# Performance work log

Hardware: AMD Instinct MI355X
Metric: run time of the kernel (lower is better)

Reference implementation:

```python
import jax, jax.numpy as jnp
import numpy as np

B, WIN, NN, NF, NH, NOUT = 4, 10, 10000, 8, 64, 1
N = B * WIN * NN          # stacked graph nodes
E = 3200000               # edges
EPS = 1e-5                # BatchNorm eps


def _gcn(x, edge_index, ew, W, b):
    # PyG GCNConv: linear first, then sym-normalized aggregation with self loops.
    xl = x @ W  # [N, H]
    loop = jnp.arange(N)
    row = jnp.concatenate([edge_index[0], loop])
    col = jnp.concatenate([edge_index[1], loop])
    w = jnp.concatenate([ew, jnp.ones((N,), ew.dtype)])
    deg = jax.ops.segment_sum(w, col, num_segments=N)
    dinv = jnp.where(deg > 0, jax.lax.rsqrt(deg), 0.0)
    norm = dinv[row] * w * dinv[col]
    out = jax.ops.segment_sum(norm[:, None] * xl[row], col, num_segments=N)
    return out + b


def _bn(x, g, bta):
    # training-mode BatchNorm1d (batch statistics, biased variance)
    m = x.mean(0)
    v = x.var(0)
    return (x - m) * jax.lax.rsqrt(v + EPS) * g + bta


def _lstm(xs, wih, whh, bih, bhh):
    # xs: [T, Bn, D]; PyTorch gate order i, f, g, o
    H = whh.shape[1]
    Bn = xs.shape[1]
    h0 = jnp.zeros((Bn, H), xs.dtype)
    c0 = jnp.zeros((Bn, H), xs.dtype)
    def step(carry, xt):
        h, c = carry
        gates = xt @ wih.T + bih + h @ whh.T + bhh
        i, f, g, o = jnp.split(gates, 4, axis=-1)
        c = jax.nn.sigmoid(f) * c + jax.nn.sigmoid(i) * jnp.tanh(g)
        h = jax.nn.sigmoid(o) * jnp.tanh(c)
        return (h, c), h
    (hn, cn), ys = jax.lax.scan(step, (h0, c0), xs)
    return ys, hn


def setup_inputs() -> dict:
    key = jax.random.key(0)
    ks = jax.random.split(key, 16)
    def rn(k, shape, s=0.05):
        return jax.random.normal(k, shape, jnp.float32) * s
    return {
        "x": jax.random.normal(ks[0], (N, NF), jnp.float32),
        "edge_index": jax.random.randint(ks[1], (2, E), 0, N),
        "edge_weight": jax.random.uniform(ks[2], (E,), jnp.float32),
        "c1_w": rn(ks[3], (NF, NH)), "c1_b": jnp.zeros((NH,), jnp.float32),
        "c2_w": rn(ks[4], (NH, NH)), "c2_b": jnp.zeros((NH,), jnp.float32),
        "bn1_g": jnp.ones((NH,), jnp.float32), "bn1_b": jnp.zeros((NH,), jnp.float32),
        "bn2_g": jnp.ones((NH,), jnp.float32), "bn2_b": jnp.zeros((NH,), jnp.float32),
        "l1_wih": rn(ks[5], (4 * NH, 2 * NH)), "l1_whh": rn(ks[6], (4 * NH, NH)),
        "l1_bih": jnp.zeros((4 * NH,), jnp.float32), "l1_bhh": jnp.zeros((4 * NH,), jnp.float32),
        "l2_wih": rn(ks[7], (4 * NH, NH)), "l2_whh": rn(ks[8], (4 * NH, NH)),
        "l2_bih": jnp.zeros((4 * NH,), jnp.float32), "l2_bhh": jnp.zeros((4 * NH,), jnp.float32),
        "fc1_w": rn(ks[9], (NH, 2 * NH + WIN * NF)), "fc1_b": jnp.zeros((NH,), jnp.float32),
        "fc2_w": rn(ks[10], (NOUT, NH)), "fc2_b": jnp.zeros((NOUT,), jnp.float32),
    }


def reference(x, edge_index, edge_weight, c1_w, c1_b, c2_w, c2_b,
              bn1_g, bn1_b, bn2_g, bn2_b,
              l1_wih, l1_whh, l1_bih, l1_bhh,
              l2_wih, l2_whh, l2_bih, l2_bhh,
              fc1_w, fc1_b, fc2_w, fc2_b):
    # skip connection: raw features per (batch,node) over the window
    skip = x.reshape(B, WIN, NN, NF).transpose(0, 2, 1, 3).reshape(B * NN, WIN * NF)
    # two GCN layers (dropout is identity in deterministic/eval reference)
    h1 = _bn(jax.nn.relu(_gcn(x, edge_index, edge_weight, c1_w, c1_b)), bn1_g, bn1_b)
    h2 = _bn(jax.nn.relu(_gcn(h1, edge_index, edge_weight, c2_w, c2_b)), bn2_g, bn2_b)
    xc = jnp.concatenate([h1, h2], axis=1)  # [N, 2H]
    xr = xc.reshape(B, WIN, NN, 2 * NH).transpose(1, 0, 2, 3).reshape(WIN, B * NN, 2 * NH)
    ys1, hn1 = _lstm(xr, l1_wih, l1_whh, l1_bih, l1_bhh)
    ys2, hn2 = _lstm(ys1, l2_wih, l2_whh, l2_bih, l2_bhh)
    z = jnp.concatenate([hn1, hn2, skip], axis=1)
    z = jax.nn.relu(z @ fc1_w.T + fc1_b)
    z = jax.nn.relu(z @ fc2_w.T + fc2_b)
    return z.reshape(-1)
```

## Files before the change

kernel.cpp:

```cpp
#include <hip/hip_runtime.h>
#include <math.h>

constexpr int BB     = 4;
constexpr int WINN   = 10;
constexpr int NNODES = 10000;
constexpr int NFEAT  = 8;
constexpr int NHID   = 64;
constexpr int NTOT   = BB * WINN * NNODES;
constexpr int NEDGE  = 3200000;
constexpr int NBN    = BB * NNODES;
constexpr float EPSBN = 1e-5f;

#define DEVFN static __device__ __forceinline__

typedef float f4 __attribute__((ext_vector_type(4)));
typedef short s8v __attribute__((ext_vector_type(8)));
typedef unsigned short ushort_t;
typedef unsigned int uint_t;

DEVFN float sigmoidf_(float x) { return 1.0f / (1.0f + __expf(-x)); }
DEVFN float tanhf_(float x) { return 2.0f / (1.0f + __expf(-2.0f * x)) - 1.0f; }
DEVFN ushort_t f2bf(float f) {
    uint_t x = __float_as_uint(f);
    return (ushort_t)((x + 0x7FFFu + ((x >> 16) & 1u)) >> 16);
}
DEVFN float bf2f(ushort_t u) { return __uint_as_float(((uint_t)u) << 16); }

__global__ void k_diag(float* out, float wsz, int n) {
    int i = blockIdx.x * 256 + threadIdx.x;
    if (i < n) out[i] = wsz;
}

__global__ void k_init(int* cntP, float* sums) {
    int i = blockIdx.x * 256 + threadIdx.x;
    if (i < 8 * NTOT) cntP[i] = 0;
    if (i < 2048) sums[i] = 0.f;
}

__global__ void k_hist(const int* __restrict__ ei, int* __restrict__ cntP) {
    int e = blockIdx.x * 256 + threadIdx.x;
    int p = blockIdx.x & 7;
    if (e < NEDGE) atomicAdd(&cntP[p * NTOT + ei[NEDGE + e]], 1);
}

__global__ void k_scan1(const int* __restrict__ cntP, int* __restrict__ ptr, int* __restrict__ tmp) {
    __shared__ int sdat[256];
    int tid = threadIdx.x;
    int base = blockIdx.x * 1024 + tid * 4;
    int v[4];
#pragma unroll
    for (int j = 0; j < 4; ++j) {
        int idx = base + j;
        int s = 0;
        if (idx < NTOT) {
#pragma unroll
            for (int p = 0; p < 8; ++p) s += cntP[p * NTOT + idx];
        }
        v[j] = s;
    }
    int sum = v[0] + v[1] + v[2] + v[3];
    sdat[tid] = sum;
    __syncthreads();
    for (int ofs = 1; ofs < 256; ofs <<= 1) {
        int x = (tid >= ofs) ? sdat[tid - ofs] : 0;
        __syncthreads();
        sdat[tid] += x;
        __syncthreads();
    }
    int run = sdat[tid] - sum;
    if (base + 0 < NTOT) ptr[base + 0] = run; run += v[0];
    if (base + 1 < NTOT) ptr[base + 1] = run; run += v[1];
    if (base + 2 < NTOT) ptr[base + 2] = run; run += v[2];
    if (base + 3 < NTOT) ptr[base + 3] = run;
    if (tid == 255) tmp[blockIdx.x] = sdat[255];
}

__global__ void k_scan2(int* tmp, int nb) {
    __shared__ int st[512];
    int tid = threadIdx.x;
    int v = (tid < nb) ? tmp[tid] : 0;
    st[tid] = v;
    __syncthreads();
    for (int ofs = 1; ofs < 512; ofs <<= 1) {
        int x = (tid >= ofs) ? st[tid - ofs] : 0;
        __syncthreads();
        st[tid] += x;
        __syncthreads();
    }
    if (tid < nb) tmp[tid] = st[tid] - v;
}

__global__ void k_scan3(int* __restrict__ ptr, int* __restrict__ cntP, const int* __restrict__ tmp) {
    int i = blockIdx.x * 256 + threadIdx.x;
    if (i < NTOT) {
        int p0 = ptr[i] + tmp[i >> 10];
        ptr[i] = p0;
        int run = p0;
#pragma unroll
        for (int p = 0; p < 8; ++p) {
            int c = cntP[p * NTOT + i];
            cntP[p * NTOT + i] = run;
            run += c;
        }
    }
    if (i == 0) ptr[NTOT] = NEDGE;
}

__global__ void k_fill(const int* __restrict__ ei, const float* __restrict__ ew,
                       int* __restrict__ cur8, int2* __restrict__ epack) {
    int e = blockIdx.x * 256 + threadIdx.x;
    if (e >= NEDGE) return;
    int p = blockIdx.x & 7;
    int row = ei[e], col = ei[NEDGE + e];
    int pos = atomicAdd(&cur8[p * NTOT + col], 1);
    epack[pos] = make_int2(row, __float_as_int(ew[e]));
}

__global__ void k_degcsr(const int* __restrict__ ptr, const int2* __restrict__ epack,
                         float* __restrict__ dinv) {
    int tid = threadIdx.x;
    int lane = tid & 63;
    int waveg = blockIdx.x * 4 + (tid >> 6);
    int g = lane >> 3, sub = lane & 7;
    int node = waveg * 8 + g;
    int beg = ptr[node], end = ptr[node + 1];
    float s = 0.f;
    for (int e = beg + sub; e < end; e += 8) s += __int_as_float(epack[e].y);
    s += __shfl_xor(s, 1, 64);
    s += __shfl_xor(s, 2, 64);
    s += __shfl_xor(s, 4, 64);
    if (sub == 0) dinv[node] = rsqrtf(1.0f + s);
}

__global__ void k_gather8(const int* __restrict__ ptr, const int2* __restrict__ epack,
                          const float* __restrict__ x, const float* __restrict__ dinv,
                          float* __restrict__ aggX) {
    int tid = threadIdx.x;
    int lane = tid & 63;
    int waveg = blockIdx.x * 4 + (tid >> 6);
    int g = lane >> 3, ch = lane & 7;
    int node = waveg * 8 + g;
    int beg = ptr[node], end = ptr[node + 1];
    float dv = dinv[node];
    float accE = 0.f;
    int e = beg;
    for (; e + 3 < end; e += 4) {
        int2 p0 = epack[e], p1 = epack[e + 1], p2 = epack[e + 2], p3 = epack[e + 3];
        float n0 = dinv[p0.x] * __int_as_float(p0.y);
        float n1 = dinv[p1.x] * __int_as_float(p1.y);
        float n2 = dinv[p2.x] * __int_as_float(p2.y);
        float n3 = dinv[p3.x] * __int_as_float(p3.y);
        accE = fmaf(n0, x[p0.x * 8 + ch], accE);
        accE = fmaf(n1, x[p1.x * 8 + ch], accE);
        accE = fmaf(n2, x[p2.x * 8 + ch], accE);
        accE = fmaf(n3, x[p3.x * 8 + ch], accE);
    }
    for (; e < end; ++e) {
        int2 p = epack[e];
        accE = fmaf(dinv[p.x] * __int_as_float(p.y), x[p.x * 8 + ch], accE);
    }
    aggX[node * 8 + ch] = dv * fmaf(dv, x[node * 8 + ch], accE);
}

__global__ void k_lin1(const float* __restrict__ aggX, const float* __restrict__ W,
                       const float* __restrict__ bias, ushort_t* __restrict__ rbf,
                       float* __restrict__ sums) {
    __shared__ float sW[NFEAT * NHID];
    int tid = threadIdx.x;
    sW[tid] = W[tid];
    sW[tid + 256] = W[tid + 256];
    __syncthreads();
    int c = tid & 63;
    float b = bias[c];
    float s = 0.f, sq = 0.f;
    int stride = gridDim.x * 256;
    for (int i = blockIdx.x * 256 + tid; i < NTOT * 64; i += stride) {
        int n = i >> 6;
        float acc = b;
#pragma unroll
        for (int f = 0; f < NFEAT; ++f) acc = fmaf(aggX[n * NFEAT + f], sW[f * NHID + c], acc);
        acc = acc > 0.f ? acc : 0.f;
        rbf[i] = f2bf(acc);
        s += acc;
        sq = fmaf(acc, acc, sq);
    }
    __shared__ float ls[4][64], lq[4][64];
    int w = tid >> 6;
    ls[w][c] = s; lq[w][c] = sq;
    __syncthreads();
    if (tid < 64) {
        atomicAdd(&sums[tid], ls[0][tid] + ls[1][tid] + ls[2][tid] + ls[3][tid]);
        atomicAdd(&sums[64 + tid], lq[0][tid] + lq[1][tid] + lq[2][tid] + lq[3][tid]);
    }
}

__global__ void k_bn_final(const float* __restrict__ sums, const float* __restrict__ g,
                           const float* __restrict__ b, float* __restrict__ ss) {
    int i = threadIdx.x;
    if (i >= 64) return;
    float mean = sums[i] * (1.0f / NTOT);
    float var = sums[64 + i] * (1.0f / NTOT) - mean * mean;
    float sc = g[i] * rsqrtf(var + EPSBN);
    ss[i] = sc;
    ss[64 + i] = b[i] - mean * sc;
}

__global__ void k_bn_final8(const float* __restrict__ sums8, const float* __restrict__ g,
                            const float* __restrict__ b, float* __restrict__ ss) {
    int i = threadIdx.x;
    if (i >= 64) return;
    float S = 0.f, Q = 0.f;
#pragma unroll
    for (int m = 0; m < 8; ++m) { S += sums8[m * 128 + i]; Q += sums8[m * 128 + 64 + i]; }
    float mean = S * (1.0f / NTOT);
    float var = Q * (1.0f / NTOT) - mean * mean;
    float sc = g[i] * rsqrtf(var + EPSBN);
    ss[i] = sc;
    ss[64 + i] = b[i] - mean * sc;
}

__global__ void k_gcn2(const int* __restrict__ ptr, const int2* __restrict__ epack,
                       const ushort_t* __restrict__ rbf, const float* __restrict__ dinv,
                       const float* __restrict__ ss1, const float* __restrict__ W2,
                       const float* __restrict__ bias2, ushort_t* __restrict__ h2bf,
                       float* __restrict__ sums8) {
    __shared__ __align__(16) float srow[4][64];
    __shared__ float ls[4][64], lq[4][64];
    int lane = threadIdx.x & 63, wv = threadIdx.x >> 6;
    float wc[64];
#pragma unroll
    for (int h = 0; h < 64; ++h) wc[h] = W2[h * 64 + lane];
    float b2v = bias2[lane];
    float sc1 = ss1[lane], sh1 = ss1[64 + lane];
    float s = 0.f, sq = 0.f;
    int wid = blockIdx.x * 4 + wv;
    int nw = gridDim.x * 4;
    for (int node = wid; node < NTOT; node += nw) {
        int beg = ptr[node], end = ptr[node + 1];
        float dv = dinv[node];
        float accE = 0.f, accS = 0.f;
        int e = beg;
        for (; e + 3 < end; e += 4) {
            int2 p0 = epack[e], p1 = epack[e + 1], p2 = epack[e + 2], p3 = epack[e + 3];
            float n0 = dinv[p0.x] * __int_as_float(p0.y);
            float n1 = dinv[p1.x] * __int_as_float(p1.y);
            float n2 = dinv[p2.x] * __int_as_float(p2.y);
            float n3 = dinv[p3.x] * __int_as_float(p3.y);
            accE = fmaf(n0, bf2f(rbf[(size_t)p0.x * 64 + lane]), accE);
            accE = fmaf(n1, bf2f(rbf[(size_t)p1.x * 64 + lane]), accE);
            accE = fmaf(n2, bf2f(rbf[(size_t)p2.x * 64 + lane]), accE);
            accE = fmaf(n3, bf2f(rbf[(size_t)p3.x * 64 + lane]), accE);
            accS += n0 + n1 + n2 + n3;
        }
        for (; e < end; ++e) {
            int2 p = epack[e];
            float nv = dinv[p.x] * __int_as_float(p.y);
            accE = fmaf(nv, bf2f(rbf[(size_t)p.x * 64 + lane]), accE);
            accS += nv;
        }
        float G = dv * fmaf(dv, bf2f(rbf[(size_t)node * 64 + lane]), accE);
        float S = dv * (dv + accS);
        srow[wv][lane] = fmaf(sc1, G, sh1 * S);
        float acc = b2v;
#pragma unroll
        for (int h4 = 0; h4 < 16; ++h4) {
            float4 iv = *reinterpret_cast<const float4*>(&srow[wv][h4 * 4]);
            acc = fmaf(iv.x, wc[h4 * 4 + 0], acc);
            acc = fmaf(iv.y, wc[h4 * 4 + 1], acc);
            acc = fmaf(iv.z, wc[h4 * 4 + 2], acc);
            acc = fmaf(iv.w, wc[h4 * 4 + 3], acc);
        }
        acc = acc > 0.f ? acc : 0.f;
        h2bf[(size_t)node * 64 + lane] = f2bf(acc);
        s += acc;
        sq = fmaf(acc, acc, sq);
    }
    ls[wv][lane] = s; lq[wv][lane] = sq;
    __syncthreads();
    if (threadIdx.x < 64) {
        float S_ = ls[0][lane] + ls[1][lane] + ls[2][lane] + ls[3][lane];
        float Q_ = lq[0][lane] + lq[1][lane] + lq[2][lane] + lq[3][lane];
        float* d = sums8 + (blockIdx.x & 7) * 128;
        atomicAdd(&d[lane], S_);
        atomicAdd(&d[64 + lane], Q_);
    }
}

__global__ void k_prep(const float* __restrict__ wih1, const float* __restrict__ whh1,
                       const float* __restrict__ bih1, const float* __restrict__ bhh1,
                       const float* __restrict__ wih2, const float* __restrict__ whh2,
                       const float* __restrict__ bih2, const float* __restrict__ bhh2,
                       const float* __restrict__ fc1w,
                       float* wB1f, float* b1, ushort_t* wB2h, float* b2, float* fc1T) {
    int i = blockIdx.x * 256 + threadIdx.x;
    if (i < 256 * 192) {
        int n = i / 192, k = i - n * 192;
        wB1f[i] = (k < 128) ? wih1[n * 128 + k] : whh1[n * 64 + (k - 128)];
    }
    if (i < 256 * 128) {
        int n = i >> 7, k = i & 127;
        wB2h[i] = f2bf((k < 64) ? wih2[n * 64 + k] : whh2[n * 64 + (k - 64)]);
    }
    if (i < 208 * 64) {
        int k = i >> 6, o = i & 63;
        fc1T[i] = fc1w[o * 208 + k];
    }
    if (i < 256) { b1[i] = bih1[i] + bhh1[i]; b2[i] = bih2[i] + bhh2[i]; }
}

__global__ void k_fold2(float* __restrict__ wB1f, float* __restrict__ b1,
                        const float* __restrict__ ss1, const float* __restrict__ ss2,
                        ushort_t* __restrict__ wB1h) {
    int n = threadIdx.x;
    float acc = 0.f;
#pragma unroll
    for (int m = 0; m < 64; ++m) {
        float w = wB1f[n * 192 + m];
        acc = fmaf(w, ss1[64 + m], acc);
        wB1f[n * 192 + m] = w * ss1[m];
    }
#pragma unroll
    for (int m = 0; m < 64; ++m) {
        float w = wB1f[n * 192 + 64 + m];
        acc = fmaf(w, ss2[64 + m], acc);
        wB1f[n * 192 + 64 + m] = w * ss2[m];
    }
    b1[n] += acc;
    __syncthreads();
    for (int j = n; j < 256 * 192; j += 256) wB1h[j] = f2bf(wB1f[j]);
}

__global__ __launch_bounds__(256, 2) void k_lstm_mfma4(
    const ushort_t* __restrict__ h1bf, const ushort_t* __restrict__ h2bf,
    const ushort_t* __restrict__ wB1, const ushort_t* __restrict__ wB2,
    const float* __restrict__ bs1, const float* __restrict__ bs2,
    float* __restrict__ hA, float* __restrict__ hB) {
    __shared__ ushort_t hx1[1024];
    __shared__ ushort_t hx2[2][1024];
    int tid = threadIdx.x;
    int lane = tid & 63, wv = tid >> 6;
    int c15 = lane & 15, g4 = lane >> 4;
    int g8 = g4 * 8;
    int bn0 = blockIdx.x * 16;
    int b = bn0 / NNODES, nn0 = bn0 - b * NNODES;

    for (int i = tid; i < 1536; i += 256) {
        if (i < 512) ((uint_t*)hx1)[i] = 0u;
        else ((uint_t*)hx2)[i - 512] = 0u;
    }

    s8v w1f[4][6], w2f[4][4];
#pragma unroll
    for (int j = 0; j < 4; ++j) {
        const ushort_t* base1 = wB1 + (size_t)((wv + 4 * j) * 16 + c15) * 192 + g8;
#pragma unroll
        for (int kk = 0; kk < 6; ++kk) w1f[j][kk] = *(const s8v*)(base1 + kk * 32);
        const ushort_t* base2 = wB2 + (size_t)((wv + 4 * j) * 16 + c15) * 128 + g8;
#pragma unroll
        for (int kk = 0; kk < 4; ++kk) w2f[j][kk] = *(const s8v*)(base2 + kk * 32);
    }
    float bi1[4], bi2[4];
#pragma unroll
    for (int j = 0; j < 4; ++j) {
        bi1[j] = bs1[(wv + 4 * j) * 16 + c15];
        bi2[j] = bs2[(wv + 4 * j) * 16 + c15];
    }
    float cA[4], cB[4];
#pragma unroll
    for (int q = 0; q < 4; ++q) { cA[q] = 0.f; cB[q] = 0.f; }

    int r7 = c15 & 7;
    int a_lo = c15 * 64 + ((g4 ^ r7) << 3);
    int a_hi = c15 * 64 + (((4 + g4) ^ r7) << 3);
    int u = wv * 16 + c15;
    int hxcol_hi = (u >> 3) << 3;
    int u7 = u & 7;

    __syncthreads();

    for (int t = 0; t < WINN; ++t) {
        size_t node = (size_t)((b * WINN + t) * NNODES + nn0 + c15) * 64 + g8;
        s8v a[6];
        a[0] = *(const s8v*)(h1bf + node);
        a[1] = *(const s8v*)(h1bf + node + 32);
        a[2] = *(const s8v*)(h2bf + node);
        a[3] = *(const s8v*)(h2bf + node + 32);
        a[4] = *(const s8v*)(&hx1[a_lo]);
        a[5] = *(const s8v*)(&hx1[a_hi]);

        f4 acc[4];
#pragma unroll
        for (int j = 0; j < 4; ++j) { f4 v = {bi1[j], bi1[j], bi1[j], bi1[j]}; acc[j] = v; }
#pragma unroll
        for (int j = 0; j < 4; ++j)
#pragma unroll
            for (int kk = 0; kk < 6; ++kk)
                acc[j] = __builtin_amdgcn_mfma_f32_16x16x32_bf16(a[kk], w1f[j][kk], acc[j], 0, 0, 0);
        __syncthreads();
#pragma unroll
        for (int q = 0; q < 4; ++q) {
            float ig = sigmoidf_(acc[0][q]);
            float fg = sigmoidf_(acc[1][q]);
            float gg = tanhf_(acc[2][q]);
            float og = sigmoidf_(acc[3][q]);
            float cv = fmaf(fg, cA[q], ig * gg);
            cA[q] = cv;
            float hv = og * tanhf_(cv);
            int rr = g4 * 4 + q;
            hx1[rr * 64 + (hxcol_hi ^ ((rr & 7) << 3)) + u7] = f2bf(hv);
        }
        __syncthreads();

        const ushort_t* hp = hx2[1 - (t & 1)];
        s8v r[4];
        r[0] = *(const s8v*)(&hx1[a_lo]);
        r[1] = *(const s8v*)(&hx1[a_hi]);
        r[2] = *(const s8v*)(&hp[a_lo]);
        r[3] = *(const s8v*)(&hp[a_hi]);
#pragma unroll
        for (int j = 0; j < 4; ++j) { f4 v = {bi2[j], bi2[j], bi2[j], bi2[j]}; acc[j] = v; }
#pragma unroll
        for (int j = 0; j < 4; ++j)
#pragma unroll
            for (int kk = 0; kk < 4; ++kk)
                acc[j] = __builtin_amdgcn_mfma_f32_16x16x32_bf16(r[kk], w2f[j][kk], acc[j], 0, 0, 0);
        ushort_t* hw = hx2[t & 1];
#pragma unroll
        for (int q = 0; q < 4; ++q) {
            float ig = sigmoidf_(acc[0][q]);
            float fg = sigmoidf_(acc[1][q]);
            float gg = tanhf_(acc[2][q]);
            float og = sigmoidf_(acc[3][q]);
            float cv = fmaf(fg, cB[q], ig * gg);
            cB[q] = cv;
            float hv = og * tanhf_(cv);
            int rr = g4 * 4 + q;
            hw[rr * 64 + (hxcol_hi ^ ((rr & 7) << 3)) + u7] = f2bf(hv);
        }
    }
    __syncthreads();
    const ushort_t* hf = hx2[(WINN - 1) & 1];
    for (int i = tid; i < 1024; i += 256) {
        int rr = i >> 6, uu = i & 63;
        int hw2 = rr * 64 + ((((uu >> 3) ^ (rr & 7)) << 3)) + (uu & 7);
        hA[(size_t)(bn0 + rr) * 64 + uu] = bf2f(hx1[hw2]);
        hB[(size_t)(bn0 + rr) * 64 + uu] = bf2f(hf[hw2]);
    }
}

__global__ void k_head(const float* __restrict__ hA, const float* __restrict__ hB,
                       const float* __restrict__ x, const float* __restrict__ fc1T,
                       const float* __restrict__ fc1b, const float* __restrict__ fc2w,
                       const float* __restrict__ fc2b, float* __restrict__ out) {
    int lane = threadIdx.x & 63, wv = threadIdx.x >> 6;
    int bn = blockIdx.x * 4 + wv;
    __shared__ float sz[4][208];
    int b = bn / NNODES, nn = bn - b * NNODES;
    for (int k = lane; k < 208; k += 64) {
        float v;
        if (k < 64) v = hA[(size_t)bn * 64 + k];
        else if (k < 128) v = hB[(size_t)bn * 64 + (k - 64)];
        else {
            int kk = k - 128;
            int w = kk >> 3, f = kk & 7;
            v = x[(size_t)((b * WINN + w) * NNODES + nn) * NFEAT + f];
        }
        sz[wv][k] = v;
    }
    __syncthreads();
    float acc = fc1b[lane];
    for (int k = 0; k < 208; ++k) acc = fmaf(sz[wv][k], fc1T[k * 64 + lane], acc);
    acc = acc > 0.f ? acc : 0.f;
    float v = acc * fc2w[lane];
#pragma unroll
    for (int m = 32; m >= 1; m >>= 1) v += __shfl_xor(v, m, 64);
    if (lane == 0) {
        float z = v + fc2b[0];
        out[bn] = z > 0.f ? z : 0.f;
    }
}

extern "C" void kernel_launch(void* const* d_in, const int* in_sizes, int n_in,
                              void* d_out, int out_size, void* d_ws, size_t ws_size,
                              hipStream_t stream) {
    const float* x     = (const float*)d_in[0];
    const int*   ei    = (const int*)d_in[1];
    const float* ew    = (const float*)d_in[2];
    const float* c1w   = (const float*)d_in[3];
    const float* c1b   = (const float*)d_in[4];
    const float* c2w   = (const float*)d_in[5];
    const float* c2b   = (const float*)d_in[6];
    const float* bn1g  = (const float*)d_in[7];
    const float* bn1b  = (const float*)d_in[8];
    const float* bn2g  = (const float*)d_in[9];
    const float* bn2b  = (const float*)d_in[10];
    const float* wih1  = (const float*)d_in[11];
    const float* whh1  = (const float*)d_in[12];
    const float* bih1  = (const float*)d_in[13];
    const float* bhh1  = (const float*)d_in[14];
    const float* wih2  = (const float*)d_in[15];
    const float* whh2  = (const float*)d_in[16];
    const float* bih2  = (const float*)d_in[17];
    const float* bhh2  = (const float*)d_in[18];
    const float* fc1w  = (const float*)d_in[19];
    const float* fc1b  = (const float*)d_in[20];
    const float* fc2w  = (const float*)d_in[21];
    const float* fc2b  = (const float*)d_in[22];
    float* out = (float*)d_out;

    float* ws = (float*)d_ws;
    size_t off = 0;
    auto A = [&](size_t n) { float* p = ws + off; off += n; return p; };
    float* dinv   = A(NTOT);
    float* aggX   = A((size_t)NTOT * NFEAT);
    ushort_t* h1bf = (ushort_t*)A((size_t)NTOT * 32);
    ushort_t* h2bf = (ushort_t*)A((size_t)NTOT * 32);

    size_t uoff = off;
    float* hA = A((size_t)NBN * 64);
    float* hB = A((size_t)NBN * 64);
    A(2 * (size_t)NEDGE + (NTOT + 1) + 8 * (size_t)NTOT - 2 * (size_t)NBN * 64);
    int2* epack = (int2*)(ws + uoff);
    int*  ptr   = (int*)(epack + NEDGE);
    int*  cntP  = ptr + NTOT + 1;

    float* wB1f = A(256 * 192);
    ushort_t* wB1h = (ushort_t*)A(256 * 96);
    ushort_t* wB2h = (ushort_t*)A(256 * 64);
    float* b1   = A(256);
    float* b2   = A(256);
    float* fc1T = A(208 * 64);
    float* sums = A(2048);
    float* ss1  = A(128);
    float* ss2  = A(128);
    float* scanTmpF = A(512);
    int* scanTmp = (int*)scanTmpF;

    if (ws_size < off * sizeof(float)) {
        k_diag<<<(out_size + 255) / 256, 256, 0, stream>>>(out, (float)ws_size, out_size);
        return;
    }

    constexpr int SCAN_NB = (NTOT + 1023) / 1024;

    k_init<<<8 * NTOT / 256, 256, 0, stream>>>(cntP, sums);
    k_hist<<<NEDGE / 256, 256, 0, stream>>>(ei, cntP);
    k_scan1<<<SCAN_NB, 256, 0, stream>>>(cntP, ptr, scanTmp);
    k_scan2<<<1, 512, 0, stream>>>(scanTmp, SCAN_NB);
    k_scan3<<<(NTOT + 255) / 256, 256, 0, stream>>>(ptr, cntP, scanTmp);
    k_fill<<<NEDGE / 256, 256, 0, stream>>>(ei, ew, cntP, epack);
    k_degcsr<<<NTOT / 8 / 4, 256, 0, stream>>>(ptr, epack, dinv);
    k_prep<<<192, 256, 0, stream>>>(wih1, whh1, bih1, bhh1, wih2, whh2, bih2, bhh2,
                                    fc1w, wB1f, b1, wB2h, b2, fc1T);

    k_gather8<<<NTOT / 8 / 4, 256, 0, stream>>>(ptr, epack, x, dinv, aggX);
    k_lin1<<<512, 256, 0, stream>>>(aggX, c1w, c1b, h1bf, sums);
    k_bn_final<<<1, 64, 0, stream>>>(sums, bn1g, bn1b, ss1);

    k_gcn2<<<2048, 256, 0, stream>>>(ptr, epack, h1bf, dinv, ss1, c2w, c2b, h2bf, sums + 128);
    k_bn_final8<<<1, 64, 0, stream>>>(sums + 128, bn2g, bn2b, ss2);
    k_fold2<<<1, 256, 0, stream>>>(wB1f, b1, ss1, ss2, wB1h);

    k_lstm_mfma4<<<NBN / 16, 256, 0, stream>>>(h1bf, h2bf, wB1h, wB2h, b1, b2, hA, hB);

    k_head<<<NBN / 4, 256, 0, stream>>>(hA, hB, x, fc1T, fc1b, fc2w, fc2b, out);
}
```

Before: 1.230 ms.

## Split GCN2 into gather and linear kernels; double-buffer LSTM layer-1 state

The fused GCN layer-2 kernel, which held 64 weight registers per lane while doing the irregular edge gather, is split in two. A lightweight one-node-per-wave gather kernel writes the normalized aggregate to a new bf16 buffer, and a separate persistent kernel applies W2, ReLU and the BN statistics. This aims to raise occupancy and latency hiding for the memory-bound gather, at the cost of an extra bf16 round trip of N×64 values and one more launch. The LSTM kernel also double-buffers the layer-1 hidden state in shared memory, which removes one __syncthreads per timestep.

Result: faster. 1.116 ms, median of 2 (-9.3%).

```diff
diff --git a/kernel.cpp b/kernel.cpp
--- a/kernel.cpp
+++ b/kernel.cpp
@@ -219,49 +219,54 @@
     ss[64 + i] = b[i] - mean * sc;
 }
 
-__global__ void k_gcn2(const int* __restrict__ ptr, const int2* __restrict__ epack,
-                       const ushort_t* __restrict__ rbf, const float* __restrict__ dinv,
-                       const float* __restrict__ ss1, const float* __restrict__ W2,
-                       const float* __restrict__ bias2, ushort_t* __restrict__ h2bf,
-                       float* __restrict__ sums8) {
+__global__ void k_gather64b(const int* __restrict__ ptr, const int2* __restrict__ epack,
+                            const ushort_t* __restrict__ rbf, const float* __restrict__ dinv,
+                            const float* __restrict__ ss1, ushort_t* __restrict__ gout) {
+    int lane = threadIdx.x & 63;
+    int node = blockIdx.x * 4 + (threadIdx.x >> 6);
+    int beg = ptr[node], end = ptr[node + 1];
+    float dv = dinv[node];
+    float accE = 0.f, accS = 0.f;
+    int e = beg;
+    for (; e + 3 < end; e += 4) {
+        int2 p0 = epack[e], p1 = epack[e + 1], p2 = epack[e + 2], p3 = epack[e + 3];
+        float n0 = dinv[p0.x] * __int_as_float(p0.y);
+        float n1 = dinv[p1.x] * __int_as_float(p1.y);
+        float n2 = dinv[p2.x] * __int_as_float(p2.y);
+        float n3 = dinv[p3.x] * __int_as_float(p3.y);
+        accE = fmaf(n0, bf2f(rbf[(size_t)p0.x * 64 + lane]), accE);
+        accE = fmaf(n1, bf2f(rbf[(size_t)p1.x * 64 + lane]), accE);
+        accE = fmaf(n2, bf2f(rbf[(size_t)p2.x * 64 + lane]), accE);
+        accE = fmaf(n3, bf2f(rbf[(size_t)p3.x * 64 + lane]), accE);
+        accS += n0 + n1 + n2 + n3;
+    }
+    for (; e < end; ++e) {
+        int2 p = epack[e];
+        float nv = dinv[p.x] * __int_as_float(p.y);
+        accE = fmaf(nv, bf2f(rbf[(size_t)p.x * 64 + lane]), accE);
+        accS += nv;
+    }
+    float G = dv * fmaf(dv, bf2f(rbf[(size_t)node * 64 + lane]), accE);
+    float S = dv * (dv + accS);
+    gout[(size_t)node * 64 + lane] = f2bf(fmaf(ss1[lane], G, ss1[64 + lane] * S));
+}
+
+__global__ void k_lin2c(const ushort_t* __restrict__ gin, const float* __restrict__ W2,
+                        const float* __restrict__ bias, ushort_t* __restrict__ dst,
+                        float* __restrict__ sums8) {
     __shared__ __align__(16) float srow[4][64];
     __shared__ float ls[4][64], lq[4][64];
     int lane = threadIdx.x & 63, wv = threadIdx.x >> 6;
     float wc[64];
 #pragma unroll
     for (int h = 0; h < 64; ++h) wc[h] = W2[h * 64 + lane];
-    float b2v = bias2[lane];
-    float sc1 = ss1[lane], sh1 = ss1[64 + lane];
+    float b = bias[lane];
     float s = 0.f, sq = 0.f;
     int wid = blockIdx.x * 4 + wv;
     int nw = gridDim.x * 4;
-    for (int node = wid; node < NTOT; node += nw) {
-        int beg = ptr[node], end = ptr[node + 1];
-        float dv = dinv[node];
-        float accE = 0.f, accS = 0.f;
-        int e = beg;
-        for (; e + 3 < end; e += 4) {
-            int2 p0 = epack[e], p1 = epack[e + 1], p2 = epack[e + 2], p3 = epack[e + 3];
-            float n0 = dinv[p0.x] * __int_as_float(p0.y);
-            float n1 = dinv[p1.x] * __int_as_float(p1.y);
-            float n2 = dinv[p2.x] * __int_as_float(p2.y);
-            float n3 = dinv[p3.x] * __int_as_float(p3.y);
-            accE = fmaf(n0, bf2f(rbf[(size_t)p0.x * 64 + lane]), accE);
-            accE = fmaf(n1, bf2f(rbf[(size_t)p1.x * 64 + lane]), accE);
-            accE = fmaf(n2, bf2f(rbf[(size_t)p2.x * 64 + lane]), accE);
-            accE = fmaf(n3, bf2f(rbf[(size_t)p3.x * 64 + lane]), accE);
-            accS += n0 + n1 + n2 + n3;
-        }
-        for (; e < end; ++e) {
-            int2 p = epack[e];
-            float nv = dinv[p.x] * __int_as_float(p.y);
-            accE = fmaf(nv, bf2f(rbf[(size_t)p.x * 64 + lane]), accE);
-            accS += nv;
-        }
-        float G = dv * fmaf(dv, bf2f(rbf[(size_t)node * 64 + lane]), accE);
-        float S = dv * (dv + accS);
-        srow[wv][lane] = fmaf(sc1, G, sh1 * S);
-        float acc = b2v;
+    for (int row = wid; row < NTOT; row += nw) {
+        srow[wv][lane] = bf2f(gin[(size_t)row * 64 + lane]);
+        float acc = b;
 #pragma unroll
         for (int h4 = 0; h4 < 16; ++h4) {
             float4 iv = *reinterpret_cast<const float4*>(&srow[wv][h4 * 4]);
@@ -271,18 +276,18 @@
             acc = fmaf(iv.w, wc[h4 * 4 + 3], acc);
         }
         acc = acc > 0.f ? acc : 0.f;
-        h2bf[(size_t)node * 64 + lane] = f2bf(acc);
+        dst[(size_t)row * 64 + lane] = f2bf(acc);
         s += acc;
         sq = fmaf(acc, acc, sq);
     }
     ls[wv][lane] = s; lq[wv][lane] = sq;
     __syncthreads();
     if (threadIdx.x < 64) {
-        float S_ = ls[0][lane] + ls[1][lane] + ls[2][lane] + ls[3][lane];
-        float Q_ = lq[0][lane] + lq[1][lane] + lq[2][lane] + lq[3][lane];
+        float S = ls[0][lane] + ls[1][lane] + ls[2][lane] + ls[3][lane];
+        float Q = lq[0][lane] + lq[1][lane] + lq[2][lane] + lq[3][lane];
         float* d = sums8 + (blockIdx.x & 7) * 128;
-        atomicAdd(&d[lane], S_);
-        atomicAdd(&d[64 + lane], Q_);
+        atomicAdd(&d[lane], S);
+        atomicAdd(&d[64 + lane], Q);
     }
 }
 
@@ -335,8 +340,7 @@
     const ushort_t* __restrict__ wB1, const ushort_t* __restrict__ wB2,
     const float* __restrict__ bs1, const float* __restrict__ bs2,
     float* __restrict__ hA, float* __restrict__ hB) {
-    __shared__ ushort_t hx1[1024];
-    __shared__ ushort_t hx2[2][1024];
+    __shared__ ushort_t hx1[2][1024], hx2[2][1024];
     int tid = threadIdx.x;
     int lane = tid & 63, wv = tid >> 6;
     int c15 = lane & 15, g4 = lane >> 4;
@@ -344,9 +348,9 @@
     int bn0 = blockIdx.x * 16;
     int b = bn0 / NNODES, nn0 = bn0 - b * NNODES;
 
-    for (int i = tid; i < 1536; i += 256) {
-        if (i < 512) ((uint_t*)hx1)[i] = 0u;
-        else ((uint_t*)hx2)[i - 512] = 0u;
+    for (int i = tid; i < 2048; i += 256) {
+        if (i < 1024) ((uint_t*)hx1)[i] = 0u;
+        else ((uint_t*)hx2)[i - 1024] = 0u;
     }
 
     s8v w1f[4][6], w2f[4][4];
@@ -379,14 +383,15 @@
     __syncthreads();
 
     for (int t = 0; t < WINN; ++t) {
+        int cur = t & 1, prv = 1 - cur;
         size_t node = (size_t)((b * WINN + t) * NNODES + nn0 + c15) * 64 + g8;
         s8v a[6];
         a[0] = *(const s8v*)(h1bf + node);
         a[1] = *(const s8v*)(h1bf + node + 32);
         a[2] = *(const s8v*)(h2bf + node);
         a[3] = *(const s8v*)(h2bf + node + 32);
-        a[4] = *(const s8v*)(&hx1[a_lo]);
-        a[5] = *(const s8v*)(&hx1[a_hi]);
+        a[4] = *(const s8v*)(&hx1[prv][a_lo]);
+        a[5] = *(const s8v*)(&hx1[prv][a_hi]);
 
         f4 acc[4];
 #pragma unroll
@@ -396,7 +401,6 @@
 #pragma unroll
             for (int kk = 0; kk < 6; ++kk)
                 acc[j] = __builtin_amdgcn_mfma_f32_16x16x32_bf16(a[kk], w1f[j][kk], acc[j], 0, 0, 0);
-        __syncthreads();
 #pragma unroll
         for (int q = 0; q < 4; ++q) {
             float ig = sigmoidf_(acc[0][q]);
@@ -407,16 +411,15 @@
             cA[q] = cv;
             float hv = og * tanhf_(cv);
             int rr = g4 * 4 + q;
-            hx1[rr * 64 + (hxcol_hi ^ ((rr & 7) << 3)) + u7] = f2bf(hv);
+            hx1[cur][rr * 64 + (hxcol_hi ^ ((rr & 7) << 3)) + u7] = f2bf(hv);
         }
         __syncthreads();
 
-        const ushort_t* hp = hx2[1 - (t & 1)];
         s8v r[4];
-        r[0] = *(const s8v*)(&hx1[a_lo]);
-        r[1] = *(const s8v*)(&hx1[a_hi]);
-        r[2] = *(const s8v*)(&hp[a_lo]);
-        r[3] = *(const s8v*)(&hp[a_hi]);
+        r[0] = *(const s8v*)(&hx1[cur][a_lo]);
+        r[1] = *(const s8v*)(&hx1[cur][a_hi]);
+        r[2] = *(const s8v*)(&hx2[prv][a_lo]);
+        r[3] = *(const s8v*)(&hx2[prv][a_hi]);
 #pragma unroll
         for (int j = 0; j < 4; ++j) { f4 v = {bi2[j], bi2[j], bi2[j], bi2[j]}; acc[j] = v; }
 #pragma unroll
@@ -424,7 +427,6 @@
 #pragma unroll
             for (int kk = 0; kk < 4; ++kk)
                 acc[j] = __builtin_amdgcn_mfma_f32_16x16x32_bf16(r[kk], w2f[j][kk], acc[j], 0, 0, 0);
-        ushort_t* hw = hx2[t & 1];
 #pragma unroll
         for (int q = 0; q < 4; ++q) {
             float ig = sigmoidf_(acc[0][q]);
@@ -435,16 +437,16 @@
             cB[q] = cv;
             float hv = og * tanhf_(cv);
             int rr = g4 * 4 + q;
-            hw[rr * 64 + (hxcol_hi ^ ((rr & 7) << 3)) + u7] = f2bf(hv);
+            hx2[cur][rr * 64 + (hxcol_hi ^ ((rr & 7) << 3)) + u7] = f2bf(hv);
         }
     }
     __syncthreads();
-    const ushort_t* hf = hx2[(WINN - 1) & 1];
+    int fin = (WINN - 1) & 1;
     for (int i = tid; i < 1024; i += 256) {
         int rr = i >> 6, uu = i & 63;
         int hw2 = rr * 64 + ((((uu >> 3) ^ (rr & 7)) << 3)) + (uu & 7);
-        hA[(size_t)(bn0 + rr) * 64 + uu] = bf2f(hx1[hw2]);
-        hB[(size_t)(bn0 + rr) * 64 + uu] = bf2f(hf[hw2]);
+        hA[(size_t)(bn0 + rr) * 64 + uu] = bf2f(hx1[fin][hw2]);
+        hB[(size_t)(bn0 + rr) * 64 + uu] = bf2f(hx2[fin][hw2]);
     }
 }
 
@@ -515,6 +517,7 @@
     float* aggX   = A((size_t)NTOT * NFEAT);
     ushort_t* h1bf = (ushort_t*)A((size_t)NTOT * 32);
     ushort_t* h2bf = (ushort_t*)A((size_t)NTOT * 32);
+    ushort_t* gbuf = (ushort_t*)A((size_t)NTOT * 32);
 
     size_t uoff = off;
     float* hA = A((size_t)NBN * 64);
@@ -557,7 +560,8 @@
     k_lin1<<<512, 256, 0, stream>>>(aggX, c1w, c1b, h1bf, sums);
     k_bn_final<<<1, 64, 0, stream>>>(sums, bn1g, bn1b, ss1);
 
-    k_gcn2<<<2048, 256, 0, stream>>>(ptr, epack, h1bf, dinv, ss1, c2w, c2b, h2bf, sums + 128);
+    k_gather64b<<<NTOT / 4, 256, 0, stream>>>(ptr, epack, h1bf, dinv, ss1, gbuf);
+    k_lin2c<<<2048, 256, 0, stream>>>(gbuf, c2w, c2b, h2bf, sums + 128);
     k_bn_final8<<<1, 64, 0, stream>>>(sums + 128, bn2g, bn2b, ss2);
     k_fold2<<<1, 256, 0, stream>>>(wB1f, b1, ss1, ss2, wB1h);
 
```
